# Kernel optimization log

Hardware: AMD Instinct MI355X
Metric: run time of the kernel (lower is better)

## Reference

```python
import jax, jax.numpy as jnp
import numpy as np
import math

EPS_BN1 = 1e-3   # batch_norm1 eps
EPS_BNP = 1e-5   # predictor BN default eps


def conv1d(x, w, b=None, stride=1, padding=0, dilation=1):
    # x: (B, Cin, T), w: (Cout, Cin, K)
    out = jax.lax.conv_general_dilated(
        x, w, window_strides=(stride,), padding=[(padding, padding)],
        rhs_dilation=(dilation,), dimension_numbers=('NCH', 'OIH', 'NCH'))
    if b is not None:
        out = out + b[None, :, None]
    return out


def bn_eval(x, g, b, m, v, eps):
    scale = g / jnp.sqrt(v + eps)
    return (x - m[None, :, None]) * scale[None, :, None] + b[None, :, None]


def setup_inputs() -> dict:
    key = jax.random.key(0)
    ks = jax.random.split(key, 16)
    B, Cin, T = 16, 256, 4096
    Cout, P = 256, 32
    f32 = jnp.float32

    def n(k, shape, s):
        return s * jax.random.normal(k, shape, dtype=f32)

    inp = {
        'x': n(ks[0], (B, Cin, T), 1.0),
        'conv1_w': n(ks[1], (2 * Cout, Cin, 1), 0.06),
        'bn1_g': 1.0 + n(ks[2], (2 * Cout,), 0.1),
        'bn1_b': n(ks[3], (2 * Cout,), 0.1),
        'bn1_m': n(ks[4], (2 * Cout,), 0.1),
        'bn1_v': 1.0 + 0.1 * jax.random.uniform(ks[5], (2 * Cout,), dtype=f32),
        'conv1x1_w': n(ks[6], (1, Cin, 1), 0.06),
        'p0_w': n(ks[7], (P, 2, 31), 0.1),
        'p0_b': n(ks[8], (P,), 0.05),
        'p0bn_g': jnp.ones((P,), f32), 'p0bn_b': jnp.zeros((P,), f32),
        'p0bn_m': n(ks[9], (P,), 0.1),
        'p0bn_v': 1.0 + 0.1 * jax.random.uniform(ks[10], (P,), dtype=f32),
        'p1_w': n(ks[11], (P, P, 15), 0.05),
        'p1_b': n(ks[12], (P,), 0.05),
        'p1bn_g': jnp.ones((P,), f32), 'p1bn_b': jnp.zeros((P,), f32),
        'p1bn_m': n(ks[13], (P,), 0.1),
        'p1bn_v': 1.0 + 0.1 * jax.random.uniform(ks[14], (P,), dtype=f32),
        # last predictor conv: weight scaled by 0.01, bias = -log(2) (per __init__)
        'p2_w': 0.01 * n(ks[15], (2, P, 15), 0.05),
        'p2_b': jnp.array([-math.log(2.0), -math.log(2.0)], dtype=f32),
        'norm_mean': jnp.ones((1,), f32),  # registered buffer, eval renorm
    }
    return inp


def _forward(x, conv1_w, bn1_g, bn1_b, bn1_m, bn1_v, conv1x1_w,
             p0_w, p0_b, p0bn_g, p0bn_b, p0bn_m, p0bn_v,
             p1_w, p1_b, p1bn_g, p1bn_b, p1bn_m, p1bn_v,
             p2_w, p2_b, norm_mean):
    B, Cin, T = x.shape
    sg = jax.lax.stop_gradient

    # conv1 -> BN -> GLU(dim=1); dropout is identity in eval
    feat = bn_eval(conv1d(x, conv1_w), bn1_g, bn1_b, bn1_m, bn1_v, EPS_BN1)
    a, g = jnp.split(feat, 2, axis=1)
    feat = a * jax.nn.sigmoid(g)                     # (B, Cout, T)

    # predictor on [__x, __x^2]
    xx = conv1d(x, conv1x1_w)                        # (B, 1, T)
    h = jnp.concatenate([xx, xx * xx], axis=1)       # (B, 2, T)
    h = jax.nn.silu(bn_eval(conv1d(h, p0_w, p0_b, padding=15),
                            p0bn_g, p0bn_b, p0bn_m, p0bn_v, EPS_BNP))
    h = jax.nn.silu(bn_eval(conv1d(h, p1_w, p1_b, padding=7),
                            p1bn_g, p1bn_b, p1bn_m, p1bn_v, EPS_BNP))
    jumps = conv1d(h, p2_w, p2_b, padding=7)         # (B, 2, T)

    weights = jax.nn.sigmoid(jumps[:, 0, :])         # (B, T)
    moves = jax.nn.sigmoid(jumps[:, 1, :]) * norm_mean[0]  # eval: renorm = norm_mean
    row_renorm = jnp.maximum(jnp.mean(moves, axis=1), 1.0)
    moves = moves / row_renorm[:, None]

    features = jnp.transpose(feat, (0, 2, 1))        # (B, T, C)
    fw = features * weights[:, :, None]

    # big_pool: poses value = cumsum(moves); grad path = local window of 21 moves
    # (the k=1..20 shift loop adds grad-only terms). Window sum via cumsum diff.
    c = jnp.cumsum(moves, axis=1)
    win = c - jnp.pad(c, ((0, 0), (21, 0)))[:, :T]   # sum of moves[i-20..i]
    poses = sg(c) + win - sg(win)                    # (B, T)

    floors = jnp.floor(poses)
    ceils = floors + 1.0
    w1 = 1.0 - (poses - floors)                      # func = line: 1 - t
    w2 = 1.0 - (ceils - poses)

    # moves <= 1 (sigmoid * norm_mean=1 / row_renorm>=1) => ceils.max()+1 <= T+2
    L = T + 2                                        # static bound for out length
    C = features.shape[2]
    bidx = jnp.arange(B)[:, None]
    fi = floors.astype(jnp.int32)
    ci = fi + 1
    out = jnp.zeros((B, L, C), dtype=features.dtype)
    out = out.at[bidx, fi].add(w1[:, :, None] * fw)
    out = out.at[bidx, ci].add(w2[:, :, None] * fw)

    x_evs = jnp.transpose(out, (0, 2, 1))            # (B, C, L)
    pad = 15 - (L % 15)                              # F.pad(0, 15 - L % 15)
    return jnp.pad(x_evs, ((0, 0), (0, 0), (0, pad)))


def reference(x, conv1_w, bn1_g, bn1_b, bn1_m, bn1_v, conv1x1_w,
              p0_w, p0_b, p0bn_g, p0bn_b, p0bn_m, p0bn_v,
              p1_w, p1_b, p1bn_g, p1bn_b, p1bn_m, p1bn_v,
              p2_w, p2_b, norm_mean):
    return _forward(x, conv1_w, bn1_g, bn1_b, bn1_m, bn1_v, conv1x1_w,
                    p0_w, p0_b, p0bn_g, p0bn_b, p0bn_m, p0bn_v,
                    p1_w, p1_b, p1bn_g, p1bn_b, p1bn_m, p1bn_v,
                    p2_w, p2_b, norm_mean)
```

## Files before the change

kernel.cpp:

```cpp
#include <hip/hip_runtime.h>
#include <hip/hip_bf16.h>

#define BB   16
#define CIN  256
#define TN   4096
#define LOUT 4110
#define FTS  4224

typedef __attribute__((ext_vector_type(8))) short s16x8;
typedef __attribute__((ext_vector_type(4))) float f32x4;


__global__ __launch_bounds__(256) void k0_prep(
    const float* __restrict__ conv1_w, const float* __restrict__ p0_w,
    const float* __restrict__ p1_w, const float* __restrict__ p2_w,
    const float* __restrict__ bn1_g, const float* __restrict__ bn1_b,
    const float* __restrict__ bn1_m, const float* __restrict__ bn1_v,
    const float* __restrict__ p0_b, const float* __restrict__ p0g,
    const float* __restrict__ p0bb, const float* __restrict__ p0m,
    const float* __restrict__ p0v,
    const float* __restrict__ p1_b, const float* __restrict__ p1g,
    const float* __restrict__ p1bb, const float* __restrict__ p1m,
    const float* __restrict__ p1v,
    short* __restrict__ wBpk, float4* __restrict__ bnp,
    float* __restrict__ wp0T, short* __restrict__ wp1M,
    short* __restrict__ wp2M, float2* __restrict__ bnp0,
    float2* __restrict__ bnp1) {
  int bid = blockIdx.x, tid = threadIdx.x;
  if (bid < 512) {
    int e = bid * 256 + tid;
    int i = e & 7, l = (e >> 3) & 63, ks = (e >> 9) & 7, n16 = e >> 12;
    int n = n16 * 16 + (l & 15);
    int j = n & 63;
    int co = (j < 32) ? ((n >> 6) * 32 + j) : (256 + (n >> 6) * 32 + (j - 32));
    int ci = ks * 32 + (l >> 4) * 8 + i;
    __hip_bfloat16 hv = __float2bfloat16(conv1_w[co * 256 + ci]);
    wBpk[e] = *(short*)&hv;
  } else {
    int idx = (bid - 512) * 256 + tid;
    if (idx < 1984) {
      int ch = idx & 31, rem = idx >> 5;
      int ic = rem / 31, k = rem % 31;
      wp0T[idx] = p0_w[(ch * 2 + ic) * 31 + k];
    }
    {
      int i = idx & 7, l = (idx >> 3) & 63, nf = (idx >> 9) & 1, koff = idx >> 10;
      int ch = nf * 16 + (l & 15), ic = (l >> 4) * 8 + i;
      __hip_bfloat16 hv = __float2bfloat16(p1_w[(ch * 32 + ic) * 15 + koff]);
      wp1M[idx] = *(short*)&hv;
    }
    if (idx < 7680) {
      int i = idx & 7, l = (idx >> 3) & 63, koff = idx >> 9;
      int n = l & 15, ic = (l >> 4) * 8 + i;
      float v = (n < 2) ? p2_w[(n * 32 + ic) * 15 + koff] : 0.f;
      __hip_bfloat16 hv = __float2bfloat16(v);
      wp2M[idx] = *(short*)&hv;
    }
    if (idx < 32) {
      int ch = idx;
      float sc = p0g[ch] * rsqrtf(p0v[ch] + 1e-5f);
      bnp0[ch] = make_float2(sc, (p0_b[ch] - p0m[ch]) * sc + p0bb[ch]);
    }
    if (idx >= 32 && idx < 64) {
      int ch = idx - 32;
      float sc = p1g[ch] * rsqrtf(p1v[ch] + 1e-5f);
      bnp1[ch] = make_float2(sc, (p1_b[ch] - p1m[ch]) * sc + p1bb[ch]);
    }
    if (idx < 256) {
      int c = idx;
      float sa = bn1_g[c] * rsqrtf(bn1_v[c] + 1e-3f);
      float ba = bn1_b[c] - bn1_m[c] * sa;
      float sg = bn1_g[c + 256] * rsqrtf(bn1_v[c + 256] + 1e-3f);
      float bg = bn1_b[c + 256] - bn1_m[c + 256] * sg;
      bnp[c] = make_float4(sa, ba, sg, bg);
    }
  }
}

__global__ __launch_bounds__(512, 4) void k1_mfma(
    const float* __restrict__ x, const float* __restrict__ w1x1,
    const short* __restrict__ wBpk, const float4* __restrict__ bnp,
    __hip_bfloat16* __restrict__ featT, float* __restrict__ xx) {
  int ty = blockIdx.x, b = blockIdx.y;
  int t0 = ty * 64;
  __shared__ float ls[64][257];
  int tid = threadIdx.x;
  const float* xb = x + (size_t)b * (CIN * TN);
#pragma unroll
  for (int s = 0; s < 8; ++s) {
    int idx = tid + s * 512;
    int ci = idx >> 4, tc = idx & 15;
    float4 v = *(const float4*)(xb + (size_t)ci * TN + t0 + tc * 4);
    ls[tc * 4 + 0][ci] = v.x;
    ls[tc * 4 + 1][ci] = v.y;
    ls[tc * 4 + 2][ci] = v.z;
    ls[tc * 4 + 3][ci] = v.w;
  }
  __syncthreads();

  {
    int t = tid >> 3, kq = tid & 7;
    float a = 0.f;
#pragma unroll 8
    for (int j = 0; j < 32; ++j)
      a = fmaf(ls[t][kq + j * 8], w1x1[kq + j * 8], a);
    a += __shfl_xor(a, 1);
    a += __shfl_xor(a, 2);
    a += __shfl_xor(a, 4);
    if (kq == 0) xx[b * TN + t0 + t] = a;
  }

  f32x4 acc[4][4];
#pragma unroll
  for (int i = 0; i < 4; ++i)
#pragma unroll
    for (int j = 0; j < 4; ++j) acc[i][j] = (f32x4){0.f, 0.f, 0.f, 0.f};

  int l = tid & 63, wv = tid >> 6;
  int lr = l & 15, lk = l >> 4;
  const short* wrow = wBpk + (size_t)l * 8;

#pragma unroll 2
  for (int ks = 0; ks < 8; ++ks) {
    s16x8 bf[4], af[4];
#pragma unroll
    for (int nf = 0; nf < 4; ++nf)
      bf[nf] = *(const s16x8*)(wrow + (size_t)(wv * 4 + nf) * 4096 + ks * 512);
#pragma unroll
    for (int mf = 0; mf < 4; ++mf) {
      const float* ap = &ls[mf * 16 + lr][ks * 32 + lk * 8];
      s16x8 t;
#pragma unroll
      for (int i = 0; i < 8; ++i) {
        __hip_bfloat16 hv = __float2bfloat16(ap[i]);
        t[i] = *(short*)&hv;
      }
      af[mf] = t;
    }
#pragma unroll
    for (int mf = 0; mf < 4; ++mf)
#pragma unroll
      for (int nf = 0; nf < 4; ++nf)
        acc[mf][nf] = __builtin_amdgcn_mfma_f32_16x16x32_bf16(
            af[mf], bf[nf], acc[mf][nf], 0, 0, 0);
  }

  int cb = wv * 32;
#pragma unroll
  for (int nf = 0; nf < 2; ++nf) {
    float4 bn = bnp[cb + nf * 16 + lr];
    int c = cb + nf * 16 + lr;
#pragma unroll
    for (int mf = 0; mf < 4; ++mf) {
#pragma unroll
      for (int r = 0; r < 4; ++r) {
        float a = acc[mf][nf][r], g = acc[mf][nf + 2][r];
        float av = fmaf(a, bn.x, bn.y);
        float gv = fmaf(g, bn.z, bn.w);
        float fv = av / (1.f + __expf(-gv));
        int t = t0 + mf * 16 + lk * 4 + r;
        featT[((size_t)b * TN + t) * 256 + c] = __float2bfloat16(fv);
      }
    }
  }
}

__global__ __launch_bounds__(512) void k2_pred(
    const float* __restrict__ xx,
    const float* __restrict__ wp0T, const float2* __restrict__ bnp0,
    const short* __restrict__ wp1M, const float2* __restrict__ bnp1,
    const short* __restrict__ wp2M, const float* __restrict__ p2_b,
    const float* __restrict__ norm_mean,
    float* __restrict__ wts, float* __restrict__ mvr) {
  int t0 = blockIdx.x * 128;
  int b = blockIdx.y;
  __shared__ float xin[2][192];
  __shared__ short h0T[160 * 40];
  __shared__ short h1T[144 * 40];
  int tid = threadIdx.x;
  for (int q = tid; q < 192; q += 512) {
    int t = t0 - 29 + q;
    float v = (q < 186 && t >= 0 && t < TN) ? xx[b * TN + t] : 0.f;
    xin[0][q] = v;
    xin[1][q] = v * v;
  }
  __syncthreads();
  {
    int ch = tid & 31, tq = tid >> 5;
    int i0 = tq * 12;
    if (i0 < 156) {
      float2 bb0 = bnp0[ch];
      float a0[12];
#pragma unroll
      for (int j = 0; j < 12; ++j) a0[j] = 0.f;
#pragma unroll
      for (int ic = 0; ic < 2; ++ic) {
        float rr[44];
#pragma unroll
        for (int q = 0; q < 11; ++q) {
          float4 t4 = *(const float4*)(&xin[ic][i0 + q * 4]);
          rr[q * 4 + 0] = t4.x; rr[q * 4 + 1] = t4.y;
          rr[q * 4 + 2] = t4.z; rr[q * 4 + 3] = t4.w;
        }
#pragma unroll
        for (int k = 0; k < 31; ++k) {
          float w = wp0T[(ic * 31 + k) * 32 + ch];
#pragma unroll
          for (int j = 0; j < 12; ++j) a0[j] = fmaf(w, rr[j + k], a0[j]);
        }
      }
#pragma unroll
      for (int j = 0; j < 12; ++j) {
        int i = i0 + j;
        if (i < 156) {
          float v = a0[j] * bb0.x + bb0.y;
          float h = v / (1.f + __expf(-v));
          __hip_bfloat16 hv = __float2bfloat16(h);
          h0T[i * 40 + ch] = *(short*)&hv;
        }
      }
    }
    if (tid < 128) h0T[(156 + (tid >> 5)) * 40 + (tid & 31)] = 0;
  }
  __syncthreads();
  int l = tid & 63, wv = tid >> 6;
  int lrow = l & 15, lk8 = (l >> 4) * 8;
  {
    f32x4 acc[2][2];
#pragma unroll
    for (int i = 0; i < 2; ++i)
#pragma unroll
      for (int j = 0; j < 2; ++j) acc[i][j] = (f32x4){0.f, 0.f, 0.f, 0.f};
    int nmf = (wv == 0) ? 2 : 1;
    for (int koff = 0; koff < 15; ++koff) {
      const short* bp = wp1M + koff * 1024;
      s16x8 bf0 = *(const s16x8*)(bp + l * 8);
      s16x8 bf1 = *(const s16x8*)(bp + 512 + l * 8);
      for (int mi = 0; mi < nmf; ++mi) {
        int mf = (mi == 0) ? wv : 8;
        s16x8 af = *(const s16x8*)(&h0T[(mf * 16 + koff + lrow) * 40 + lk8]);
        acc[mi][0] = __builtin_amdgcn_mfma_f32_16x16x32_bf16(af, bf0, acc[mi][0], 0, 0, 0);
        acc[mi][1] = __builtin_amdgcn_mfma_f32_16x16x32_bf16(af, bf1, acc[mi][1], 0, 0, 0);
      }
    }
    for (int mi = 0; mi < nmf; ++mi) {
      int mf = (mi == 0) ? wv : 8;
#pragma unroll
      for (int nf = 0; nf < 2; ++nf) {
        int ch = nf * 16 + lrow;
        float2 bb = bnp1[ch];
#pragma unroll
        for (int r = 0; r < 4; ++r) {
          int row = mf * 16 + (l >> 4) * 4 + r;
          float v = acc[mi][nf][r] * bb.x + bb.y;
          float h = v / (1.f + __expf(-v));
          __hip_bfloat16 hv = __float2bfloat16(h);
          h1T[row * 40 + ch] = *(short*)&hv;
        }
      }
    }
  }
  __syncthreads();
  {
    f32x4 acc2 = (f32x4){0.f, 0.f, 0.f, 0.f};
    for (int koff = 0; koff < 15; ++koff) {
      s16x8 bf = *(const s16x8*)(wp2M + koff * 512 + l * 8);
      s16x8 af = *(const s16x8*)(&h1T[(wv * 16 + koff + lrow) * 40 + lk8]);
      acc2 = __builtin_amdgcn_mfma_f32_16x16x32_bf16(af, bf, acc2, 0, 0, 0);
    }
    int ch = lrow;
    if (ch < 2) {
      float pb = p2_b[ch];
      float nm = norm_mean[0];
#pragma unroll
      for (int r = 0; r < 4; ++r) {
        int t = t0 + wv * 16 + (l >> 4) * 4 + r;
        float a = acc2[r] + pb;
        float s = 1.f / (1.f + __expf(-a));
        if (ch == 0) wts[b * TN + t] = s;
        else         mvr[b * TN + t] = s * nm;
      }
    }
  }
}

__global__ __launch_bounds__(256) void k3_scan(const float* __restrict__ mvr,
                                               float* __restrict__ poses,
                                               int* __restrict__ firstT) {
  int b = blockIdx.x, tid = threadIdx.x;
  __shared__ float csum[256];
  __shared__ int shlast;
  float v[16];
  const float* src = mvr + b * TN + tid * 16;
  float run = 0.f;
#pragma unroll
  for (int j = 0; j < 16; ++j) { run += src[j]; v[j] = run; }
  csum[tid] = run;
  __syncthreads();
  for (int off = 1; off < 256; off <<= 1) {
    float tv = (tid >= off) ? csum[tid - off] : 0.f;
    __syncthreads();
    csum[tid] += tv;
    __syncthreads();
  }
  float incl = csum[tid];
  float total = csum[255];
  float excl = incl - run;
  __syncthreads();
  float rn = total * (1.0f / 4096.0f);
  float inv = (rn > 1.0f) ? 1.0f / rn : 1.0f;
  float p16[16];
  float* pd = poses + b * TN + tid * 16;
#pragma unroll
  for (int j = 0; j < 16; ++j) { p16[j] = (excl + v[j]) * inv; pd[j] = p16[j]; }
  csum[tid] = p16[15];
  __syncthreads();
  int* ft = firstT + b * FTS;
  int prevf = (tid == 0) ? -1 : min((int)floorf(csum[tid - 1]), 4220);
  int f = prevf;
#pragma unroll
  for (int j = 0; j < 16; ++j) {
    f = min((int)floorf(p16[j]), 4220);
    for (int l = prevf + 1; l <= f; ++l) ft[l] = tid * 16 + j;
    prevf = f;
  }
  if (tid == 255) shlast = f;
  __syncthreads();
  for (int l = shlast + 1 + tid; l < FTS; l += 256) ft[l] = TN;
}

__global__ __launch_bounds__(256) void k4_gather(
    const __hip_bfloat16* __restrict__ featT, const float* __restrict__ wts,
    const float* __restrict__ poses, const int* __restrict__ firstT,
    float* __restrict__ out) {
  int d = blockIdx.x + 257 * blockIdx.y;
  int w = (d & 7) * 514 + (d >> 3);
  int lx = w % 257, b = w / 257;
  int l0 = lx * 16;
  __shared__ float acc[16][259];
  int tid = threadIdx.x;
  for (int i = tid; i < 16 * 259; i += 256) ((float*)acc)[i] = 0.f;
  const int* ft = firstT + b * FTS;
  int ts = (l0 == 0) ? 0 : ft[l0 - 1];
  int te = ft[l0 + 16];
  __syncthreads();
  int c = tid;
  if (ts < te) {
    const float* pp = poses + b * TN;
    const float* wp = wts + b * TN;
    const __hip_bfloat16* fp = featT + (size_t)(b * TN) * 256 + c;
    float p_cur = pp[ts];
    float w_cur = wp[ts];
    float f_cur = __bfloat162float(fp[(size_t)ts * 256]);
    float S_lo = 0.f, S_hi = 0.f;
    int cur = (int)floorf(p_cur);
    for (int t = ts; t < te; ++t) {
      float p_nxt = 0.f, w_nxt = 0.f, f_nxt = 0.f;
      if (t + 1 < te) {
        p_nxt = pp[t + 1];
        w_nxt = wp[t + 1];
        f_nxt = __bfloat162float(fp[(size_t)(t + 1) * 256]);
      }
      int fi = (int)floorf(p_cur);
      if (fi < cur) fi = cur;
      if (fi != cur) {
        int r = cur - l0;
        if (r >= 0 && r < 16) acc[r][c] = S_lo;
        if (fi == cur + 1) {
          S_lo = S_hi;
        } else {
          int r2 = cur + 1 - l0;
          if (r2 >= 0 && r2 < 16) acc[r2][c] = S_hi;
          S_lo = 0.f;
        }
        S_hi = 0.f;
        cur = fi;
      }
      float w2 = p_cur - (float)fi;
      float fw = f_cur * w_cur;
      S_lo = fmaf(1.f - w2, fw, S_lo);
      S_hi = fmaf(w2, fw, S_hi);
      p_cur = p_nxt; w_cur = w_nxt; f_cur = f_nxt;
    }
    int r = cur - l0;
    if (r >= 0 && r < 16) acc[r][c] = S_lo;
    int r2 = cur + 1 - l0;
    if (r2 >= 0 && r2 < 16) acc[r2][c] = S_hi;
  }
  __syncthreads();
  for (int i = tid; i < 4096; i += 256) {
    int c2 = i >> 4, r = i & 15;
    int l = l0 + r;
    if (l < LOUT) out[((size_t)b * 256 + c2) * LOUT + l] = acc[r][c2];
  }
}

extern "C" void kernel_launch(void* const* d_in, const int* in_sizes, int n_in,
                              void* d_out, int out_size, void* d_ws, size_t ws_size,
                              hipStream_t stream) {
  const float* x       = (const float*)d_in[0];
  const float* conv1_w = (const float*)d_in[1];
  const float* bn1_g   = (const float*)d_in[2];
  const float* bn1_b   = (const float*)d_in[3];
  const float* bn1_m   = (const float*)d_in[4];
  const float* bn1_v   = (const float*)d_in[5];
  const float* w1x1    = (const float*)d_in[6];
  const float* p0_w    = (const float*)d_in[7];
  const float* p0_b    = (const float*)d_in[8];
  const float* p0g     = (const float*)d_in[9];
  const float* p0bb    = (const float*)d_in[10];
  const float* p0m     = (const float*)d_in[11];
  const float* p0v     = (const float*)d_in[12];
  const float* p1_w    = (const float*)d_in[13];
  const float* p1_b    = (const float*)d_in[14];
  const float* p1g     = (const float*)d_in[15];
  const float* p1bb    = (const float*)d_in[16];
  const float* p1m     = (const float*)d_in[17];
  const float* p1v     = (const float*)d_in[18];
  const float* p2_w    = (const float*)d_in[19];
  const float* p2_b    = (const float*)d_in[20];
  const float* nmean   = (const float*)d_in[21];

  char* ws = (char*)d_ws;
  __hip_bfloat16* featT = (__hip_bfloat16*)ws;
  short* wBpk   = (short*)(ws + 33554432);
  float4* bnp   = (float4*)(ws + 33816576);
  float* wp0T   = (float*)(ws + 33820672);
  short* wp1M   = (short*)(ws + 33828864);
  short* wp2M   = (short*)(ws + 33859584);
  float2* bnp0  = (float2*)(ws + 33874944);
  float2* bnp1  = (float2*)(ws + 33875200);
  float* xx     = (float*)(ws + 33890304);
  float* wts    = (float*)(ws + 34152448);
  float* mvr    = (float*)(ws + 34414592);
  float* poses  = (float*)(ws + 34676736);
  int*   firstT = (int*)  (ws + 34938880);
  float* out    = (float*)d_out;

  k0_prep<<<dim3(572), dim3(256), 0, stream>>>(
      conv1_w, p0_w, p1_w, p2_w, bn1_g, bn1_b, bn1_m, bn1_v,
      p0_b, p0g, p0bb, p0m, p0v, p1_b, p1g, p1bb, p1m, p1v,
      wBpk, bnp, wp0T, wp1M, wp2M, bnp0, bnp1);
  k1_mfma<<<dim3(64, 16), dim3(512), 0, stream>>>(x, w1x1, wBpk, bnp, featT, xx);
  k2_pred<<<dim3(32, 16), dim3(512), 0, stream>>>(xx, wp0T, bnp0, wp1M, bnp1,
                                                  wp2M, p2_b, nmean, wts, mvr);
  k3_scan<<<dim3(16), dim3(256), 0, stream>>>(mvr, poses, firstT);
  k4_gather<<<dim3(257, 16), dim3(256), 0, stream>>>(featT, wts, poses, firstT, out);
}
```

Before: 98.49 us.

## Split GLU conv GEMM across XCD-grouped blocks with bf16 swizzled LDS staging

The input-projection kernel now launches four 256-thread blocks per 64-timestep tile instead of one 512-thread block. Each block computes one quarter of the output channels. Block IDs are remapped so that the four blocks sharing a tile land on the same XCD, which should let their repeated reads of x be served from that XCD's L2. The x tile is converted to bf16 once and packed into XOR-swizzled LDS, replacing per-fragment fp32-to-bf16 conversion from a padded fp32 array. This also roughly halves LDS use, which should help occupancy. The trade-off is that each x tile is fetched four times and the conv1x1 reduction is computed redundantly in every block.

Result: faster. 95.59 us (-2.9%).

```diff
diff --git a/kernel.cpp b/kernel.cpp
--- a/kernel.cpp
+++ b/kernel.cpp
@@ -77,90 +77,95 @@
   }
 }
 
-__global__ __launch_bounds__(512, 4) void k1_mfma(
+__global__ __launch_bounds__(256, 4) void k1_mfma(
     const float* __restrict__ x, const float* __restrict__ w1x1,
     const short* __restrict__ wBpk, const float4* __restrict__ bnp,
     __hip_bfloat16* __restrict__ featT, float* __restrict__ xx) {
-  int ty = blockIdx.x, b = blockIdx.y;
+  int bid = blockIdx.x;
+  int xcd = bid & 7, kk = bid >> 3;
+  int nblk = kk & 3;
+  int T = (kk >> 2) * 8 + xcd;
+  int ty = T & 63, b = T >> 6;
   int t0 = ty * 64;
-  __shared__ float ls[64][257];
+  __shared__ __align__(16) unsigned int hb[64 * 132];
+  __shared__ float xws[4][68];
   int tid = threadIdx.x;
-  const float* xb = x + (size_t)b * (CIN * TN);
-#pragma unroll
-  for (int s = 0; s < 8; ++s) {
-    int idx = tid + s * 512;
-    int ci = idx >> 4, tc = idx & 15;
-    float4 v = *(const float4*)(xb + (size_t)ci * TN + t0 + tc * 4);
-    ls[tc * 4 + 0][ci] = v.x;
-    ls[tc * 4 + 1][ci] = v.y;
-    ls[tc * 4 + 2][ci] = v.z;
-    ls[tc * 4 + 3][ci] = v.w;
-  }
-  __syncthreads();
-
-  {
-    int t = tid >> 3, kq = tid & 7;
-    float a = 0.f;
-#pragma unroll 8
-    for (int j = 0; j < 32; ++j)
-      a = fmaf(ls[t][kq + j * 8], w1x1[kq + j * 8], a);
-    a += __shfl_xor(a, 1);
-    a += __shfl_xor(a, 2);
-    a += __shfl_xor(a, 4);
-    if (kq == 0) xx[b * TN + t0 + t] = a;
-  }
-
-  f32x4 acc[4][4];
-#pragma unroll
-  for (int i = 0; i < 4; ++i)
-#pragma unroll
-    for (int j = 0; j < 4; ++j) acc[i][j] = (f32x4){0.f, 0.f, 0.f, 0.f};
-
   int l = tid & 63, wv = tid >> 6;
+  int tq = l & 15, Cb = l >> 4;
+  int q = (tq >> 1) & 3;
+  const float* xb = x + (size_t)b * (CIN * TN) + t0 + 4 * tq;
+  float xxp[4] = {0.f, 0.f, 0.f, 0.f};
+#pragma unroll 2
+  for (int iter = 0; iter < 8; ++iter) {
+    int C = 4 * wv + Cb + 16 * iter;
+    int ci = 2 * C;
+    float4 f0 = *(const float4*)(xb + (size_t)ci * TN);
+    float4 f1 = *(const float4*)(xb + (size_t)(ci + 1) * TN);
+    float w0 = w1x1[ci], w1 = w1x1[ci + 1];
+    unsigned int* dst = hb + (C ^ (q << 2));
+    float fa[4] = {f0.x, f0.y, f0.z, f0.w};
+    float fb[4] = {f1.x, f1.y, f1.z, f1.w};
+#pragma unroll
+    for (int r = 0; r < 4; ++r) {
+      __hip_bfloat16 lo = __float2bfloat16(fa[r]);
+      __hip_bfloat16 hi = __float2bfloat16(fb[r]);
+      unsigned int pk = (unsigned int)(*(unsigned short*)&lo) |
+                        ((unsigned int)(*(unsigned short*)&hi) << 16);
+      dst[(4 * tq + r) * 132] = pk;
+      xxp[r] = fmaf(w0, fa[r], fmaf(w1, fb[r], xxp[r]));
+    }
+  }
+#pragma unroll
+  for (int r = 0; r < 4; ++r) {
+    xxp[r] += __shfl_xor(xxp[r], 16);
+    xxp[r] += __shfl_xor(xxp[r], 32);
+  }
+  if (Cb == 0) {
+#pragma unroll
+    for (int r = 0; r < 4; ++r) xws[wv][4 * tq + r] = xxp[r];
+  }
+  __syncthreads();
+  if (tid < 64)
+    xx[b * TN + t0 + tid] = xws[0][tid] + xws[1][tid] + xws[2][tid] + xws[3][tid];
+
+  f32x4 acc[4][2];
+#pragma unroll
+  for (int i = 0; i < 4; ++i) {
+    acc[i][0] = (f32x4){0.f, 0.f, 0.f, 0.f};
+    acc[i][1] = (f32x4){0.f, 0.f, 0.f, 0.f};
+  }
   int lr = l & 15, lk = l >> 4;
+  int glu = 2 * nblk + (wv >> 1), sub = wv & 1;
+  int n16a = glu * 4 + sub;
   const short* wrow = wBpk + (size_t)l * 8;
 
 #pragma unroll 2
   for (int ks = 0; ks < 8; ++ks) {
-    s16x8 bf[4], af[4];
-#pragma unroll
-    for (int nf = 0; nf < 4; ++nf)
-      bf[nf] = *(const s16x8*)(wrow + (size_t)(wv * 4 + nf) * 4096 + ks * 512);
+    s16x8 bf0 = *(const s16x8*)(wrow + (size_t)n16a * 4096 + ks * 512);
+    s16x8 bf1 = *(const s16x8*)(wrow + (size_t)(n16a + 2) * 4096 + ks * 512);
 #pragma unroll
     for (int mf = 0; mf < 4; ++mf) {
-      const float* ap = &ls[mf * 16 + lr][ks * 32 + lk * 8];
-      s16x8 t;
-#pragma unroll
-      for (int i = 0; i < 8; ++i) {
-        __hip_bfloat16 hv = __float2bfloat16(ap[i]);
-        t[i] = *(short*)&hv;
-      }
-      af[mf] = t;
-    }
-#pragma unroll
-    for (int mf = 0; mf < 4; ++mf)
-#pragma unroll
-      for (int nf = 0; nf < 4; ++nf)
-        acc[mf][nf] = __builtin_amdgcn_mfma_f32_16x16x32_bf16(
-            af[mf], bf[nf], acc[mf][nf], 0, 0, 0);
-  }
-
-  int cb = wv * 32;
-#pragma unroll
-  for (int nf = 0; nf < 2; ++nf) {
-    float4 bn = bnp[cb + nf * 16 + lr];
-    int c = cb + nf * 16 + lr;
-#pragma unroll
-    for (int mf = 0; mf < 4; ++mf) {
-#pragma unroll
-      for (int r = 0; r < 4; ++r) {
-        float a = acc[mf][nf][r], g = acc[mf][nf + 2][r];
-        float av = fmaf(a, bn.x, bn.y);
-        float gv = fmaf(g, bn.z, bn.w);
-        float fv = av / (1.f + __expf(-gv));
-        int t = t0 + mf * 16 + lk * 4 + r;
-        featT[((size_t)b * TN + t) * 256 + c] = __float2bfloat16(fv);
-      }
+      int row = mf * 16 + lr;
+      int grp = ks * 4 + lk;
+      int qr = (row >> 3) & 3;
+      s16x8 af = *(const s16x8*)(hb + row * 132 + ((grp ^ qr) << 2));
+      acc[mf][0] = __builtin_amdgcn_mfma_f32_16x16x32_bf16(af, bf0, acc[mf][0], 0, 0, 0);
+      acc[mf][1] = __builtin_amdgcn_mfma_f32_16x16x32_bf16(af, bf1, acc[mf][1], 0, 0, 0);
+    }
+  }
+
+  int c = glu * 32 + sub * 16 + lr;
+  float4 bn = bnp[c];
+#pragma unroll
+  for (int mf = 0; mf < 4; ++mf) {
+#pragma unroll
+    for (int r = 0; r < 4; ++r) {
+      float a = acc[mf][0][r], g = acc[mf][1][r];
+      float av = fmaf(a, bn.x, bn.y);
+      float gv = fmaf(g, bn.z, bn.w);
+      float fv = av / (1.f + __expf(-gv));
+      int t = t0 + mf * 16 + lk * 4 + r;
+      featT[((size_t)b * TN + t) * 256 + c] = __float2bfloat16(fv);
     }
   }
 }
@@ -441,7 +446,7 @@
       conv1_w, p0_w, p1_w, p2_w, bn1_g, bn1_b, bn1_m, bn1_v,
       p0_b, p0g, p0bb, p0m, p0v, p1_b, p1g, p1bb, p1m, p1v,
       wBpk, bnp, wp0T, wp1M, wp2M, bnp0, bnp1);
-  k1_mfma<<<dim3(64, 16), dim3(512), 0, stream>>>(x, w1x1, wBpk, bnp, featT, xx);
+  k1_mfma<<<dim3(4096), dim3(256), 0, stream>>>(x, w1x1, wBpk, bnp, featT, xx);
   k2_pred<<<dim3(32, 16), dim3(512), 0, stream>>>(xx, wp0T, bnp0, wp1M, bnp1,
                                                   wp2M, p2_b, nmean, wts, mvr);
   k3_scan<<<dim3(16), dim3(256), 0, stream>>>(mvr, poses, firstT);
```
